# Kernel optimization log

Measured on AMD Instinct MI355X. Metric: run time of the kernel, lower is better.

The kernel has to match this reference:

```python
import jax, jax.numpy as jnp
import numpy as np

B, T, H, OUT_STEPS, D = 131072, 51, 64, 20, 4


def setup_inputs() -> dict:
    key = jax.random.key(0)
    ks = jax.random.split(key, 11)
    s = 1.0 / np.sqrt(H)  # torch nn.GRU / nn.Linear uniform init bound
    u = lambda k, shape: jax.random.uniform(k, shape, jnp.float32, -s, s)
    return {
        "input_seq": jax.random.normal(ks[0], (B, T, D), jnp.float32),
        "enc_Wih": u(ks[1], (3 * H, D)),
        "enc_Whh": u(ks[2], (3 * H, H)),
        "enc_bih": u(ks[3], (3 * H,)),
        "enc_bhh": u(ks[4], (3 * H,)),
        "dec_Wih": u(ks[5], (3 * H, D)),
        "dec_Whh": u(ks[6], (3 * H, H)),
        "dec_bih": u(ks[7], (3 * H,)),
        "dec_bhh": u(ks[8], (3 * H,)),
        "lin_W": u(ks[9], (D, H)),
        "lin_b": u(ks[10], (D,)),
    }


def _gru_cell(x, h, Wih, Whh, bih, bhh):
    """PyTorch GRU cell semantics. x: [B,D_in], h: [B,H]."""
    gi = x @ Wih.T + bih  # [B,3H]
    gh = h @ Whh.T + bhh  # [B,3H]
    ir, iz, inn = jnp.split(gi, 3, axis=-1)
    hr, hz, hn = jnp.split(gh, 3, axis=-1)
    r = jax.nn.sigmoid(ir + hr)
    z = jax.nn.sigmoid(iz + hz)
    n = jnp.tanh(inn + r * hn)
    return (1.0 - z) * n + z * h


def reference(input_seq, enc_Wih, enc_Whh, enc_bih, enc_bhh,
              dec_Wih, dec_Whh, dec_bih, dec_bhh, lin_W, lin_b):
    # offset: last observed point, broadcast over the 20 output steps
    offset = input_seq[:, -1:, :]  # [B,1,D]
    diffs = input_seq[:, 1:] - input_seq[:, :-1]  # [B,T-1,D]; dropout p=0 -> identity
    h0 = jnp.zeros((input_seq.shape[0], H), input_seq.dtype)

    def enc_step(h, x_t):
        return _gru_cell(x_t, h, enc_Wih, enc_Whh, enc_bih, enc_bhh), None

    hn, _ = jax.lax.scan(enc_step, h0, jnp.swapaxes(diffs, 0, 1))  # final hidden [B,H]

    def dec_step(carry, _):
        h, px = carry
        h = _gru_cell(px, h, dec_Wih, dec_Whh, dec_bih, dec_bhh)
        x = h @ lin_W.T + lin_b + px  # linear + residual
        return (h, x), x

    _, xs = jax.lax.scan(dec_step, (hn, diffs[:, -1]), None, length=OUT_STEPS)
    out = jnp.swapaxes(xs, 0, 1)  # [B,OUT_STEPS,D]
    return out + offset
```

## Files before the change

kernel.cpp:

```cpp
#include <hip/hip_runtime.h>
#include <hip/hip_bf16.h>

namespace {

constexpr int kT = 51;
constexpr int kOut = 20;
constexpr float kL2E  = 1.4426950408889634f;
constexpr float kL2E2 = 2.8853900817779268f;

typedef __attribute__((ext_vector_type(8))) short bf16x8;
typedef __attribute__((ext_vector_type(4))) float f32x4;

union FragU {
    bf16x8 v;
    unsigned long long u64[2];
    unsigned int u32[4];
    unsigned short s[8];
};

__device__ __forceinline__ unsigned short f2bf(float x) {
    union { float f; unsigned int u; } v;
    v.f = x;
    unsigned int r = (v.u + 0x7fffu + ((v.u >> 16) & 1u)) >> 16;
    return (unsigned short)r;
}

__device__ __forceinline__ unsigned int packbf(float a, float b) {
    union { float f; unsigned int u; } ua, ub;
    ua.f = a; ub.f = b;
    return __builtin_amdgcn_perm(ub.u + 0x8000u, ua.u + 0x8000u, 0x07060302u);
}

__global__ __launch_bounds__(256, 2) void gru_encdec(
    const float* __restrict__ input,
    const float* __restrict__ eWih, const float* __restrict__ eWhh,
    const float* __restrict__ ebih, const float* __restrict__ ebhh,
    const float* __restrict__ dWih, const float* __restrict__ dWhh,
    const float* __restrict__ dbih, const float* __restrict__ dbhh,
    const float* __restrict__ linW, const float* __restrict__ linb,
    float* __restrict__ out)
{
    __shared__ __align__(16) unsigned short hlds[4][16 * 68];
    __shared__ __align__(16) float sout[4][16 * 84];

    const int lane = (int)(threadIdx.x & 63u);
    const int wid = (int)(threadIdx.x >> 6u);
    const int q = lane >> 4;
    const int i = lane & 15;
    const long b = (long)blockIdx.x * 64 + wid * 16 + i;
    const float* __restrict__ xrow = input + b * (kT * 4);
    unsigned short* __restrict__ hl = hlds[wid];
    float* __restrict__ so = sout[wid];

    bf16x8 WA[12][2];
    bf16x8 WAUG[12];
    f32x4 bhhn4[4];
    float hprev[16];
    bf16x8 bh0 = {0, 0, 0, 0, 0, 0, 0, 0};
    bf16x8 bh1 = {0, 0, 0, 0, 0, 0, 0, 0};
    float px[4];
    const f32x4 z4 = {0.f, 0.f, 0.f, 0.f};
    const bool q0 = (q == 0);

    auto load_whh = [&](const float* __restrict__ Whh) {
#pragma unroll
        for (int tau = 0; tau < 12; ++tau) {
            const float sc = (tau < 8) ? kL2E : kL2E2;
#pragma unroll
            for (int f = 0; f < 2; ++f) {
                const float* p = Whh + (tau * 16 + i) * 64 + f * 32 + q * 8;
                FragU fu;
#pragma unroll
                for (int j = 0; j < 8; ++j) fu.s[j] = f2bf(p[j] * sc);
                WA[tau][f] = fu.v;
            }
        }
    };

    auto load_aug = [&](const float* __restrict__ Wih,
                        const float* __restrict__ bih,
                        const float* __restrict__ bhh) {
#pragma unroll
        for (int tau = 0; tau < 12; ++tau) {
            const float sc = (tau < 8) ? kL2E : kL2E2;
            FragU fu;
            fu.u64[0] = 0; fu.u64[1] = 0;
            if (q0) {
                int j = tau * 16 + i;
#pragma unroll
                for (int d = 0; d < 4; ++d) fu.s[d] = f2bf(Wih[j * 4 + d] * sc);
                float bias = (tau < 8) ? (bih[j] + bhh[j]) : bih[j];
                fu.s[4] = f2bf(bias * sc);
            }
            WAUG[tau] = fu.v;
        }
#pragma unroll
        for (int t = 0; t < 4; ++t)
#pragma unroll
            for (int r = 0; r < 4; ++r)
                bhhn4[t][r] = bhh[128 + 16 * t + 4 * q + r] * kL2E2;
    };

    auto make_baug = [&]() -> bf16x8 {
        FragU fu;
        unsigned int p01 = packbf(px[0], px[1]);
        unsigned int p23 = packbf(px[2], px[3]);
        fu.u32[0] = q0 ? p01 : 0u;
        fu.u32[1] = q0 ? p23 : 0u;
        fu.u32[2] = q0 ? 0x3f80u : 0u;
        fu.u32[3] = 0u;
        return fu.v;
    };

    auto gru_step = [&](bf16x8 baug) {
#pragma unroll
        for (int t = 0; t < 4; ++t) {
            f32x4 accR = __builtin_amdgcn_mfma_f32_16x16x32_bf16(WAUG[t], baug, z4, 0, 0, 0);
            accR = __builtin_amdgcn_mfma_f32_16x16x32_bf16(WA[t][0], bh0, accR, 0, 0, 0);
            accR = __builtin_amdgcn_mfma_f32_16x16x32_bf16(WA[t][1], bh1, accR, 0, 0, 0);
            f32x4 accZ = __builtin_amdgcn_mfma_f32_16x16x32_bf16(WAUG[4 + t], baug, z4, 0, 0, 0);
            accZ = __builtin_amdgcn_mfma_f32_16x16x32_bf16(WA[4 + t][0], bh0, accZ, 0, 0, 0);
            accZ = __builtin_amdgcn_mfma_f32_16x16x32_bf16(WA[4 + t][1], bh1, accZ, 0, 0, 0);
            f32x4 accNi = __builtin_amdgcn_mfma_f32_16x16x32_bf16(WAUG[8 + t], baug, z4, 0, 0, 0);
            f32x4 accNh = __builtin_amdgcn_mfma_f32_16x16x32_bf16(WA[8 + t][0], bh0, bhhn4[t], 0, 0, 0);
            accNh = __builtin_amdgcn_mfma_f32_16x16x32_bf16(WA[8 + t][1], bh1, accNh, 0, 0, 0);

            float hv[4];
#pragma unroll
            for (int r = 0; r < 4; ++r) {
                float rr = __builtin_amdgcn_rcpf(1.f + __builtin_amdgcn_exp2f(-accR[r]));
                float zz = __builtin_amdgcn_rcpf(1.f + __builtin_amdgcn_exp2f(-accZ[r]));
                float pre2 = __builtin_fmaf(rr, accNh[r], accNi[r]);
                float tt = __builtin_amdgcn_rcpf(__builtin_amdgcn_exp2f(pre2) + 1.f);
                float nn = __builtin_fmaf(-2.f, tt, 1.f);
                float hp = hprev[t * 4 + r];
                hv[r] = __builtin_fmaf(zz, hp - nn, nn);
                hprev[t * 4 + r] = hv[r];
            }
            uint2 wv;
            wv.x = packbf(hv[0], hv[1]);
            wv.y = packbf(hv[2], hv[3]);
            *(uint2*)&hl[i * 68 + 16 * t + 4 * q] = wv;
        }
        FragU f0, f1;
        f0.u64[0] = *(const unsigned long long*)&hl[i * 68 + 8 * q];
        f0.u64[1] = *(const unsigned long long*)&hl[i * 68 + 8 * q + 4];
        f1.u64[0] = *(const unsigned long long*)&hl[i * 68 + 32 + 8 * q];
        f1.u64[1] = *(const unsigned long long*)&hl[i * 68 + 32 + 8 * q + 4];
        bh0 = f0.v;
        bh1 = f1.v;
    };

#pragma unroll
    for (int t = 0; t < 16; ++t) hprev[t] = 0.f;
    load_whh(eWhh);
    load_aug(eWih, ebih, ebhh);

    float4 xp = *(const float4*)(xrow);
    float4 xn = *(const float4*)(xrow + 4);
#pragma unroll 1
    for (int s = 0; s < kT - 1; ++s) {
        int idx = s + 2; if (idx > kT - 1) idx = kT - 1;
        float4 xf = *(const float4*)(xrow + idx * 4);
        px[0] = xn.x - xp.x;
        px[1] = xn.y - xp.y;
        px[2] = xn.z - xp.z;
        px[3] = xn.w - xp.w;
        gru_step(make_baug());
        xp = xn;
        xn = xf;
    }
    float4 offv = xp;

    load_whh(dWhh);
    load_aug(dWih, dbih, dbhh);

    bf16x8 AL0, AL1, AL2;
    {
        FragU a0, a1, a2;
        a0.u64[0] = a0.u64[1] = 0;
        a1.u64[0] = a1.u64[1] = 0;
        a2.u64[0] = a2.u64[1] = 0;
        if (i < 4) {
            const float* p0 = linW + i * 64 + q * 8;
            const float* p1 = linW + i * 64 + 32 + q * 8;
#pragma unroll
            for (int j = 0; j < 8; ++j) {
                a0.s[j] = f2bf(p0[j]);
                a1.s[j] = f2bf(p1[j]);
            }
            if (q0) a2.s[4] = f2bf(linb[i]);
        }
        AL0 = a0.v; AL1 = a1.v; AL2 = a2.v;
    }

#pragma unroll 1
    for (int s = 0; s < kOut; ++s) {
        bf16x8 baug = make_baug();
        gru_step(baug);
        f32x4 accX = __builtin_amdgcn_mfma_f32_16x16x32_bf16(AL2, baug, z4, 0, 0, 0);
        accX = __builtin_amdgcn_mfma_f32_16x16x32_bf16(AL0, bh0, accX, 0, 0, 0);
        accX = __builtin_amdgcn_mfma_f32_16x16x32_bf16(AL1, bh1, accX, 0, 0, 0);
        if (q0) {
            float x0 = accX[0] + px[0];
            float x1 = accX[1] + px[1];
            float x2 = accX[2] + px[2];
            float x3 = accX[3] + px[3];
            float* sr = so + i * 84 + s * 4;
            sr[0] = x0 + offv.x;
            sr[1] = x1 + offv.y;
            sr[2] = x2 + offv.z;
            sr[3] = x3 + offv.w;
            px[0] = x0; px[1] = x1; px[2] = x2; px[3] = x3;
        }
    }

    {
        float* __restrict__ go = out + ((long)blockIdx.x * 64 + wid * 16) * (kOut * 4);
#pragma unroll
        for (int it = 0; it < 5; ++it) {
            int g = it * 256 + lane * 4;
            int row = g / 80;
            int e = g - row * 80;
            float4 v = *(const float4*)&so[row * 84 + e];
            *(float4*)&go[g] = v;
        }
    }
}

}

extern "C" void kernel_launch(void* const* d_in, const int* in_sizes, int n_in,
                              void* d_out, int out_size, void* d_ws, size_t ws_size,
                              hipStream_t stream) {
    const float* input = (const float*)d_in[0];
    const float* eWih = (const float*)d_in[1];
    const float* eWhh = (const float*)d_in[2];
    const float* ebih = (const float*)d_in[3];
    const float* ebhh = (const float*)d_in[4];
    const float* dWih = (const float*)d_in[5];
    const float* dWhh = (const float*)d_in[6];
    const float* dbih = (const float*)d_in[7];
    const float* dbhh = (const float*)d_in[8];
    const float* linW = (const float*)d_in[9];
    const float* linb = (const float*)d_in[10];
    float* out = (float*)d_out;

    const int B = in_sizes[0] / (kT * 4);
    const int nblocks = B / 64;
    gru_encdec<<<nblocks, 256, 0, stream>>>(input, eWih, eWhh, ebih, ebhh,
                                            dWih, dWhh, dbih, dbhh,
                                            linW, linb, out);
}
```

Measured before the change: 753.3 us.

## Split GRU hidden units across wave pairs with double-buffered shared hidden state

Each 16-row batch tile is now handled by two waves, each computing half of the hidden units (6 of 12 gate tiles), instead of one wave doing all 12. The waves exchange their halves of the hidden state through a double-buffered LDS buffer with a block-wide barrier every step. The block covers 32 rows instead of 64, and launch bounds rise to 3 blocks per CU because per-wave register use is roughly halved. This shortens the serial MFMA and activation chain per recurrent step and raises occupancy. In exchange it adds a __syncthreads per timestep, redundant decoder output math in both waves, and twice as many blocks.

```diff
diff --git a/kernel.cpp b/kernel.cpp
--- a/kernel.cpp
+++ b/kernel.cpp
@@ -31,7 +31,7 @@
     return __builtin_amdgcn_perm(ub.u + 0x8000u, ua.u + 0x8000u, 0x07060302u);
 }
 
-__global__ __launch_bounds__(256, 2) void gru_encdec(
+__global__ __launch_bounds__(256, 3) void gru_encdec(
     const float* __restrict__ input,
     const float* __restrict__ eWih, const float* __restrict__ eWhh,
     const float* __restrict__ ebih, const float* __restrict__ ebhh,
@@ -40,39 +40,46 @@
     const float* __restrict__ linW, const float* __restrict__ linb,
     float* __restrict__ out)
 {
-    __shared__ __align__(16) unsigned short hlds[4][16 * 68];
-    __shared__ __align__(16) float sout[4][16 * 84];
+    __shared__ __align__(16) unsigned short hbuf[2][2][16 * 68];
+    __shared__ __align__(16) float sout[2][16 * 84];
 
     const int lane = (int)(threadIdx.x & 63u);
     const int wid = (int)(threadIdx.x >> 6u);
+    const int p = wid >> 1;
+    const int w = wid & 1;
     const int q = lane >> 4;
     const int i = lane & 15;
-    const long b = (long)blockIdx.x * 64 + wid * 16 + i;
+    const long b = (long)blockIdx.x * 32 + p * 16 + i;
     const float* __restrict__ xrow = input + b * (kT * 4);
-    unsigned short* __restrict__ hl = hlds[wid];
-    float* __restrict__ so = sout[wid];
-
-    bf16x8 WA[12][2];
-    bf16x8 WAUG[12];
-    f32x4 bhhn4[4];
-    float hprev[16];
+    const bool q0 = (q == 0);
+
+    bf16x8 WA[6][2];
+    bf16x8 WAUG[6];
+    f32x4 bhhn4[2];
+    float hprev[8];
     bf16x8 bh0 = {0, 0, 0, 0, 0, 0, 0, 0};
     bf16x8 bh1 = {0, 0, 0, 0, 0, 0, 0, 0};
     float px[4];
     const f32x4 z4 = {0.f, 0.f, 0.f, 0.f};
-    const bool q0 = (q == 0);
+    int sel = 0;
+
+    auto gtile = [&](int l) -> int {
+        return (l < 2) ? (2 * w + l) : (l < 4) ? (4 + 2 * w + l - 2)
+                                               : (8 + 2 * w + l - 4);
+    };
 
     auto load_whh = [&](const float* __restrict__ Whh) {
 #pragma unroll
-        for (int tau = 0; tau < 12; ++tau) {
-            const float sc = (tau < 8) ? kL2E : kL2E2;
+        for (int l = 0; l < 6; ++l) {
+            const int tau = gtile(l);
+            const float sc = (l < 4) ? kL2E : kL2E2;
 #pragma unroll
             for (int f = 0; f < 2; ++f) {
-                const float* p = Whh + (tau * 16 + i) * 64 + f * 32 + q * 8;
+                const float* ptr = Whh + (tau * 16 + i) * 64 + f * 32 + q * 8;
                 FragU fu;
 #pragma unroll
-                for (int j = 0; j < 8; ++j) fu.s[j] = f2bf(p[j] * sc);
-                WA[tau][f] = fu.v;
+                for (int j = 0; j < 8; ++j) fu.s[j] = f2bf(ptr[j] * sc);
+                WA[l][f] = fu.v;
             }
         }
     };
@@ -81,24 +88,25 @@
                         const float* __restrict__ bih,
                         const float* __restrict__ bhh) {
 #pragma unroll
-        for (int tau = 0; tau < 12; ++tau) {
-            const float sc = (tau < 8) ? kL2E : kL2E2;
+        for (int l = 0; l < 6; ++l) {
+            const int tau = gtile(l);
+            const float sc = (l < 4) ? kL2E : kL2E2;
             FragU fu;
             fu.u64[0] = 0; fu.u64[1] = 0;
             if (q0) {
                 int j = tau * 16 + i;
 #pragma unroll
                 for (int d = 0; d < 4; ++d) fu.s[d] = f2bf(Wih[j * 4 + d] * sc);
-                float bias = (tau < 8) ? (bih[j] + bhh[j]) : bih[j];
+                float bias = (l < 4) ? (bih[j] + bhh[j]) : bih[j];
                 fu.s[4] = f2bf(bias * sc);
             }
-            WAUG[tau] = fu.v;
-        }
-#pragma unroll
-        for (int t = 0; t < 4; ++t)
+            WAUG[l] = fu.v;
+        }
+#pragma unroll
+        for (int t = 0; t < 2; ++t)
 #pragma unroll
             for (int r = 0; r < 4; ++r)
-                bhhn4[t][r] = bhh[128 + 16 * t + 4 * q + r] * kL2E2;
+                bhhn4[t][r] = bhh[128 + 32 * w + 16 * t + 4 * q + r] * kL2E2;
     };
 
     auto make_baug = [&]() -> bf16x8 {
@@ -113,17 +121,18 @@
     };
 
     auto gru_step = [&](bf16x8 baug) {
-#pragma unroll
-        for (int t = 0; t < 4; ++t) {
+        unsigned short* __restrict__ hw = hbuf[p][sel];
+#pragma unroll
+        for (int t = 0; t < 2; ++t) {
             f32x4 accR = __builtin_amdgcn_mfma_f32_16x16x32_bf16(WAUG[t], baug, z4, 0, 0, 0);
             accR = __builtin_amdgcn_mfma_f32_16x16x32_bf16(WA[t][0], bh0, accR, 0, 0, 0);
             accR = __builtin_amdgcn_mfma_f32_16x16x32_bf16(WA[t][1], bh1, accR, 0, 0, 0);
-            f32x4 accZ = __builtin_amdgcn_mfma_f32_16x16x32_bf16(WAUG[4 + t], baug, z4, 0, 0, 0);
-            accZ = __builtin_amdgcn_mfma_f32_16x16x32_bf16(WA[4 + t][0], bh0, accZ, 0, 0, 0);
-            accZ = __builtin_amdgcn_mfma_f32_16x16x32_bf16(WA[4 + t][1], bh1, accZ, 0, 0, 0);
-            f32x4 accNi = __builtin_amdgcn_mfma_f32_16x16x32_bf16(WAUG[8 + t], baug, z4, 0, 0, 0);
-            f32x4 accNh = __builtin_amdgcn_mfma_f32_16x16x32_bf16(WA[8 + t][0], bh0, bhhn4[t], 0, 0, 0);
-            accNh = __builtin_amdgcn_mfma_f32_16x16x32_bf16(WA[8 + t][1], bh1, accNh, 0, 0, 0);
+            f32x4 accZ = __builtin_amdgcn_mfma_f32_16x16x32_bf16(WAUG[2 + t], baug, z4, 0, 0, 0);
+            accZ = __builtin_amdgcn_mfma_f32_16x16x32_bf16(WA[2 + t][0], bh0, accZ, 0, 0, 0);
+            accZ = __builtin_amdgcn_mfma_f32_16x16x32_bf16(WA[2 + t][1], bh1, accZ, 0, 0, 0);
+            f32x4 accNi = __builtin_amdgcn_mfma_f32_16x16x32_bf16(WAUG[4 + t], baug, z4, 0, 0, 0);
+            f32x4 accNh = __builtin_amdgcn_mfma_f32_16x16x32_bf16(WA[4 + t][0], bh0, bhhn4[t], 0, 0, 0);
+            accNh = __builtin_amdgcn_mfma_f32_16x16x32_bf16(WA[4 + t][1], bh1, accNh, 0, 0, 0);
 
             float hv[4];
 #pragma unroll
@@ -140,19 +149,21 @@
             uint2 wv;
             wv.x = packbf(hv[0], hv[1]);
             wv.y = packbf(hv[2], hv[3]);
-            *(uint2*)&hl[i * 68 + 16 * t + 4 * q] = wv;
-        }
+            *(uint2*)&hw[i * 68 + 32 * w + 16 * t + 4 * q] = wv;
+        }
+        __syncthreads();
         FragU f0, f1;
-        f0.u64[0] = *(const unsigned long long*)&hl[i * 68 + 8 * q];
-        f0.u64[1] = *(const unsigned long long*)&hl[i * 68 + 8 * q + 4];
-        f1.u64[0] = *(const unsigned long long*)&hl[i * 68 + 32 + 8 * q];
-        f1.u64[1] = *(const unsigned long long*)&hl[i * 68 + 32 + 8 * q + 4];
+        f0.u64[0] = *(const unsigned long long*)&hw[i * 68 + 8 * q];
+        f0.u64[1] = *(const unsigned long long*)&hw[i * 68 + 8 * q + 4];
+        f1.u64[0] = *(const unsigned long long*)&hw[i * 68 + 32 + 8 * q];
+        f1.u64[1] = *(const unsigned long long*)&hw[i * 68 + 32 + 8 * q + 4];
         bh0 = f0.v;
         bh1 = f1.v;
-    };
-
-#pragma unroll
-    for (int t = 0; t < 16; ++t) hprev[t] = 0.f;
+        sel ^= 1;
+    };
+
+#pragma unroll
+    for (int t = 0; t < 8; ++t) hprev[t] = 0.f;
     load_whh(eWhh);
     load_aug(eWih, ebih, ebhh);
 
@@ -193,6 +204,7 @@
         }
         AL0 = a0.v; AL1 = a1.v; AL2 = a2.v;
     }
+    float* __restrict__ so = sout[p];
 
 #pragma unroll 1
     for (int s = 0; s < kOut; ++s) {
@@ -201,22 +213,22 @@
         f32x4 accX = __builtin_amdgcn_mfma_f32_16x16x32_bf16(AL2, baug, z4, 0, 0, 0);
         accX = __builtin_amdgcn_mfma_f32_16x16x32_bf16(AL0, bh0, accX, 0, 0, 0);
         accX = __builtin_amdgcn_mfma_f32_16x16x32_bf16(AL1, bh1, accX, 0, 0, 0);
-        if (q0) {
-            float x0 = accX[0] + px[0];
-            float x1 = accX[1] + px[1];
-            float x2 = accX[2] + px[2];
-            float x3 = accX[3] + px[3];
+        float x0 = accX[0] + px[0];
+        float x1 = accX[1] + px[1];
+        float x2 = accX[2] + px[2];
+        float x3 = accX[3] + px[3];
+        if (w == 0 && q0) {
             float* sr = so + i * 84 + s * 4;
             sr[0] = x0 + offv.x;
             sr[1] = x1 + offv.y;
             sr[2] = x2 + offv.z;
             sr[3] = x3 + offv.w;
-            px[0] = x0; px[1] = x1; px[2] = x2; px[3] = x3;
-        }
-    }
-
-    {
-        float* __restrict__ go = out + ((long)blockIdx.x * 64 + wid * 16) * (kOut * 4);
+        }
+        px[0] = x0; px[1] = x1; px[2] = x2; px[3] = x3;
+    }
+
+    if (w == 0) {
+        float* __restrict__ go = out + ((long)blockIdx.x * 32 + p * 16) * (kOut * 4);
 #pragma unroll
         for (int it = 0; it < 5; ++it) {
             int g = it * 256 + lane * 4;
@@ -247,7 +259,7 @@
     float* out = (float*)d_out;
 
     const int B = in_sizes[0] / (kT * 4);
-    const int nblocks = B / 64;
+    const int nblocks = B / 32;
     gru_encdec<<<nblocks, 256, 0, stream>>>(input, eWih, eWhh, ebih, ebhh,
                                             dWih, dWhh, dbih, dbhh,
                                             linW, linb, out);
```

After: 686.0 us. 1.1x faster.
